# Optimization experiments

Hardware: AMD Instinct MI355X
Metric: run time of the kernel (lower is better)

Reference implementation:

```python
import jax, jax.numpy as jnp
import numpy as np

EPS = 1e-5

def _offset_conv(x, w, b):
    # 3x3 conv, padding=1, producing 2*K*K offset channels (standard DeformConv2D v1)
    out = jax.lax.conv_general_dilated(x, w, (1, 1), ((1, 1), (1, 1)),
                                       dimension_numbers=('NCHW', 'OIHW', 'NCHW'))
    return out + b[None, :, None, None]

def _bilinear_gather(x, py, px):
    # x: [B,C,H,W]; py,px: [B,K2,H,W] float sample coords -> [B,C,K2,H,W]
    B, C, H, W = x.shape
    py = jnp.clip(py, 0.0, H - 1.0)
    px = jnp.clip(px, 0.0, W - 1.0)
    y0 = jnp.floor(py)
    x0 = jnp.floor(px)
    wy = py - y0
    wx = px - x0
    y0i = y0.astype(jnp.int32)
    x0i = x0.astype(jnp.int32)
    y1i = jnp.minimum(y0i + 1, H - 1)
    x1i = jnp.minimum(x0i + 1, W - 1)
    xf = x.reshape(B, C, H * W)
    K2, Ho, Wo = py.shape[1], py.shape[2], py.shape[3]
    def gather(yy, xx):
        idx = (yy * W + xx).reshape(B, 1, -1)  # broadcast over C
        return jnp.take_along_axis(xf, idx, axis=2).reshape(B, C, K2, Ho, Wo)
    v00 = gather(y0i, x0i)
    v01 = gather(y0i, x1i)
    v10 = gather(y1i, x0i)
    v11 = gather(y1i, x1i)
    wy = wy[:, None]
    wx = wx[:, None]
    return (v00 * (1 - wy) * (1 - wx) + v01 * (1 - wy) * wx
            + v10 * wy * (1 - wx) + v11 * wy * wx)

def _deform_dw(x, w_off, b_off, w_dw, k):
    # depthwise deformable conv, kernel k, padding k//2 (same spatial size)
    B, C, H, W = x.shape
    K2 = k * k
    off = _offset_conv(x, w_off, b_off)      # [B, 2*K2, H, W]
    dy, dx = off[:, :K2], off[:, K2:]
    r = (k - 1) // 2
    pn = jnp.arange(-r, r + 1, dtype=x.dtype)
    pn_y = jnp.repeat(pn, k)[None, :, None, None]  # [1,K2,1,1]
    pn_x = jnp.tile(pn, k)[None, :, None, None]
    gy = jnp.arange(H, dtype=x.dtype)[None, None, :, None]
    gx = jnp.arange(W, dtype=x.dtype)[None, None, None, :]
    py = gy + pn_y + dy
    px = gx + pn_x + dx
    samp = _bilinear_gather(x, py, px)        # [B,C,K2,H,W]
    return jnp.einsum('bckhw,ck->bchw', samp, w_dw.reshape(C, K2))

def _bn_relu(x, g, b, m, v):
    inv = g / jnp.sqrt(v + EPS)
    return jax.nn.relu(x * inv[None, :, None, None] + (b - m * inv)[None, :, None, None])

def setup_inputs() -> dict:
    key = jax.random.key(0)
    B, C, H, W, O = 4, 96, 64, 64, 192
    ks = jax.random.split(key, 32)
    d = {'x': jax.random.normal(ks[0], (B, C, H, W), jnp.float32)}
    i = 1
    for k in (3, 5, 7):
        K2 = k * k
        d[f'w_off{k}'] = 0.01 * jax.random.normal(ks[i], (2 * K2, C, 3, 3), jnp.float32); i += 1
        d[f'b_off{k}'] = jnp.zeros((2 * K2,), jnp.float32)
        d[f'w_dw{k}'] = jax.random.normal(ks[i], (C, k, k), jnp.float32) / k; i += 1
        d[f'g{k}'] = jnp.ones((C,), jnp.float32)
        d[f'be{k}'] = jnp.zeros((C,), jnp.float32)
        d[f'm{k}'] = 0.1 * jax.random.normal(ks[i], (C,), jnp.float32); i += 1
        d[f'v{k}'] = jax.random.uniform(ks[i], (C,), jnp.float32, 0.5, 1.5); i += 1
    d['w_pw'] = jax.random.normal(ks[i], (O, 3 * C), jnp.float32) / np.sqrt(3 * C).astype(np.float32); i += 1
    d['gp'] = jnp.ones((O,), jnp.float32)
    d['bp'] = jnp.zeros((O,), jnp.float32)
    d['mp'] = 0.1 * jax.random.normal(ks[i], (O,), jnp.float32); i += 1
    d['vp'] = jax.random.uniform(ks[i], (O,), jnp.float32, 0.5, 1.5)
    return d

def reference(x, w_off3, b_off3, w_dw3, g3, be3, m3, v3,
              w_off5, b_off5, w_dw5, g5, be5, m5, v5,
              w_off7, b_off7, w_dw7, g7, be7, m7, v7,
              w_pw, gp, bp, mp, vp):
    x1 = _bn_relu(_deform_dw(x, w_off3, b_off3, w_dw3, 3), g3, be3, m3, v3)
    x2 = _bn_relu(_deform_dw(x, w_off5, b_off5, w_dw5, 5), g5, be5, m5, v5)
    x3 = _bn_relu(_deform_dw(x, w_off7, b_off7, w_dw7, 7), g7, be7, m7, v7)
    xc = jnp.concatenate([x1, x2, x3], axis=1)  # [B, 3C, H, W]
    out = jnp.einsum('bchw,oc->bohw', xc, w_pw)  # 1x1 conv
    return _bn_relu(out, gp, bp, mp, vp)
```

## Files before the change

### kernel.cpp

```cpp
#include <hip/hip_runtime.h>
#include <hip/hip_fp16.h>
#include <math.h>

typedef unsigned short u16;
typedef _Float16 f16x8 __attribute__((ext_vector_type(8)));
typedef float f32x4 __attribute__((ext_vector_type(4)));

#define HWp 4096
#define Cc 96
#define Bb 4
#define Oo 192
#define C3 288

#define OFF_WDWT  0
#define OFF_BCAT  14112
#define OFF_SBR   14304
#define OFF_HBR   14592
#define OFF_SPW   14880
#define OFF_HPW   15072
#define FP32_END  15264
#define BF_XTPAD  0
#define BF_WOF    1672704
#define BF_WPW    1838592

__device__ __forceinline__ u16 f2h(float f) { return __half_as_ushort(__float2half(f)); }
__device__ __forceinline__ float h2f(u16 u) { union { __half h; u16 u; } t; t.u = u; return __half2float(t.h); }
__device__ __forceinline__ unsigned h2u(__half2 h) { union { __half2 h; unsigned u; } t; t.h = h; return t.u; }
__device__ __forceinline__ __half2 u2h(unsigned u) { union { __half2 h; unsigned u; } t; t.u = u; return t.h; }

#define PREP_N (165888 + 55296 + 14112 + 192 + 288 + 288 + 192 + 192 + 24960)
#define PREP_BLK ((PREP_N + 255) / 256)

__global__ __launch_bounds__(256) void prep_kernel(
    const float* __restrict__ x,
    const float* __restrict__ w3, const float* __restrict__ b3, const float* __restrict__ dw3,
    const float* __restrict__ g3, const float* __restrict__ be3, const float* __restrict__ m3, const float* __restrict__ v3,
    const float* __restrict__ w5, const float* __restrict__ b5, const float* __restrict__ dw5,
    const float* __restrict__ g5, const float* __restrict__ be5, const float* __restrict__ m5, const float* __restrict__ v5,
    const float* __restrict__ w7, const float* __restrict__ b7, const float* __restrict__ dw7,
    const float* __restrict__ g7, const float* __restrict__ be7, const float* __restrict__ m7, const float* __restrict__ v7,
    const float* __restrict__ wpw,
    const float* __restrict__ gp, const float* __restrict__ bp, const float* __restrict__ mp, const float* __restrict__ vp,
    float* __restrict__ ws)
{
    __shared__ u16 sT[64 * 104];
    u16* bf = (u16*)(ws + FP32_END);
    const int tid = threadIdx.x;

    if (blockIdx.x < 256) {
        const int b = blockIdx.x >> 6, h = blockIdx.x & 63;
        const float* xb = x + (((size_t)b * Cc) << 12) + (h << 6);
#pragma unroll
        for (int it = 0; it < 24; ++it) {
            int j = tid + it * 256;
            int c = j >> 6, p = j & 63;
            sT[p * 104 + c] = f2h(xb[((size_t)c << 12) + p]);
        }
        __syncthreads();
        u16* dst = bf + BF_XTPAD + ((size_t)(b * 66 + h + 1) * 66 + 1) * 96;
#pragma unroll
        for (int it = 0; it < 6; ++it) {
            int j = tid + it * 256;
            int pos = j / 24, c4 = j % 24;
            const u16* s = &sT[pos * 104 + c4 * 4];
            *(uint2*)(dst + pos * 96 + c4 * 4) = make_uint2(
                (unsigned)s[0] | ((unsigned)s[1] << 16),
                (unsigned)s[2] | ((unsigned)s[3] << 16));
        }
        return;
    }

    int i = (blockIdx.x - 256) * 256 + tid;
    if (i < 165888) {
        int f = i / 13824, r = i % 13824;
        int s = r >> 9, l = r & 511;
        int lane = l >> 3, j = l & 7;
        int o = f * 16 + (lane & 15);
        int k = s * 32 + (lane >> 4) * 8 + j;
        int tap = k / 96, c = k % 96;
        float v = 0.f;
        if (o < 18)       v = w3[o * 864 + c * 9 + tap];
        else if (o < 68)  v = w5[(o - 18) * 864 + c * 9 + tap];
        else if (o < 166) v = w7[(o - 68) * 864 + c * 9 + tap];
        bf[BF_WOF + i] = f2h(v);
        return;
    }
    int j = i - 165888;
    if (j < 55296) {
        int f = j / 4608, r = j % 4608;
        int s = r >> 9, l = r & 511;
        int lane = l >> 3, jj = l & 7;
        int o = f * 16 + (lane & 15);
        int k = s * 32 + (lane >> 4) * 8 + jj;
        bf[BF_WPW + j] = f2h(wpw[o * C3 + k]);
        return;
    }
    j -= 55296;
    if (j < 14112) {
        int ksel = j / 4704, rem = j % 4704;
        int t = rem / 96, c = rem % 96;
        int K2 = (ksel == 0) ? 9 : (ksel == 1) ? 25 : 49;
        const float* dw = (ksel == 0) ? dw3 : (ksel == 1) ? dw5 : dw7;
        ws[OFF_WDWT + j] = (t < K2) ? dw[c * K2 + t] : 0.f;
        return;
    }
    j -= 14112;
    if (j < 192) {
        float v = 0.f;
        if (j < 18)       v = b3[j];
        else if (j < 68)  v = b5[j - 18];
        else if (j < 166) v = b7[j - 68];
        ws[OFF_BCAT + j] = v;
        return;
    }
    j -= 192;
    if (j < C3) {
        int ks = j / Cc, c = j % Cc;
        const float* g = (ks == 0) ? g3 : (ks == 1) ? g5 : g7;
        const float* v = (ks == 0) ? v3 : (ks == 1) ? v5 : v7;
        ws[OFF_SBR + j] = g[c] / sqrtf(v[c] + 1e-5f);
        return;
    }
    j -= C3;
    if (j < C3) {
        int ks = j / Cc, c = j % Cc;
        const float* g = (ks == 0) ? g3 : (ks == 1) ? g5 : g7;
        const float* v = (ks == 0) ? v3 : (ks == 1) ? v5 : v7;
        const float* be = (ks == 0) ? be3 : (ks == 1) ? be5 : be7;
        const float* m = (ks == 0) ? m3 : (ks == 1) ? m5 : m7;
        float inv = g[c] / sqrtf(v[c] + 1e-5f);
        ws[OFF_HBR + j] = be[c] - m[c] * inv;
        return;
    }
    j -= C3;
    if (j < Oo) { ws[OFF_SPW + j] = gp[j] / sqrtf(vp[j] + 1e-5f); return; }
    j -= Oo;
    if (j < Oo) {
        float inv = gp[j] / sqrtf(vp[j] + 1e-5f);
        ws[OFF_HPW + j] = bp[j] - mp[j] * inv;
        return;
    }
    j -= Oo;
    if (j < 24960) {
        int c4 = j % 24, rem = j / 24;
        int cell = rem % 260, bb = rem / 260;
        int row, col;
        if (cell < 66)       { row = 0;  col = cell; }
        else if (cell < 132) { row = 65; col = cell - 66; }
        else if (cell < 196) { row = cell - 132 + 1; col = 0; }
        else                 { row = cell - 196 + 1; col = 65; }
        u16* dst = bf + BF_XTPAD + ((size_t)(bb * 66 + row) * 66 + col) * 96 + c4 * 4;
        *(uint2*)dst = make_uint2(0u, 0u);
        return;
    }
}

#define GATHER_TAP(SEG, T, GT) do {                                          \
    const uint4 e = sWI[((GT) << 4) + q];                                    \
    const __half2 wAh = u2h(e.x), wBh = u2h(e.y);                            \
    const __half2 w00b = __low2half2(wAh), w01b = __high2half2(wAh);         \
    const __half2 w10b = __low2half2(wBh), w11b = __high2half2(wBh);         \
    const unsigned d01 = e.w & 0xffffu, d10 = e.w >> 16;                     \
    const uint4 u00 = *(const uint4*)(xcb + e.z);                            \
    const uint4 u01 = *(const uint4*)(xcb + e.z + d01);                      \
    const uint4 u10 = *(const uint4*)(xcb + e.z + d10);                      \
    const uint4 u11 = *(const uint4*)(xcb + e.z + d10 + d01);                \
    const float4 wda = *(const float4*)(wdT##SEG + (T) * 96);                \
    const float4 wdb = *(const float4*)(wdT##SEG + (T) * 96 + 4);            \
    const unsigned a00[4] = {u00.x, u00.y, u00.z, u00.w};                    \
    const unsigned a01[4] = {u01.x, u01.y, u01.z, u01.w};                    \
    const unsigned a10[4] = {u10.x, u10.y, u10.z, u10.w};                    \
    const unsigned a11[4] = {u11.x, u11.y, u11.z, u11.w};                    \
    const float wd[8] = {wda.x, wda.y, wda.z, wda.w, wdb.x, wdb.y, wdb.z, wdb.w}; \
    _Pragma("unroll")                                                        \
    for (int d = 0; d < 4; ++d) {                                            \
        __half2 v = __hmul2(w00b, u2h(a00[d]));                              \
        v = __hfma2(w01b, u2h(a01[d]), v);                                   \
        v = __hfma2(w10b, u2h(a10[d]), v);                                   \
        v = __hfma2(w11b, u2h(a11[d]), v);                                   \
        acc##SEG[2 * d]     = fmaf(wd[2 * d],     __low2float(v),  acc##SEG[2 * d]);     \
        acc##SEG[2 * d + 1] = fmaf(wd[2 * d + 1], __high2float(v), acc##SEG[2 * d + 1]); \
    }                                                                        \
} while (0)

#define SEG_EPI(SEG) do {                                                    \
    const int cb = (SEG) * Cc + c;                                           \
    const float4 sa = *(const float4*)(ws + OFF_SBR + cb);                   \
    const float4 sb = *(const float4*)(ws + OFF_SBR + cb + 4);               \
    const float4 ha = *(const float4*)(ws + OFF_HBR + cb);                   \
    const float4 hb = *(const float4*)(ws + OFF_HBR + cb + 4);               \
    const float ss[8] = {sa.x, sa.y, sa.z, sa.w, sb.x, sb.y, sb.z, sb.w};    \
    const float hh8[8] = {ha.x, ha.y, ha.z, ha.w, hb.x, hb.y, hb.z, hb.w};   \
    unsigned rr[4];                                                          \
    _Pragma("unroll")                                                        \
    for (int d = 0; d < 4; ++d) {                                            \
        float lo = fmaxf(fmaf(acc##SEG[2 * d],     ss[2 * d],     hh8[2 * d]),     0.f); \
        float hi = fmaxf(fmaf(acc##SEG[2 * d + 1], ss[2 * d + 1], hh8[2 * d + 1]), 0.f); \
        rr[d] = h2u(__floats2half2_rn(lo, hi));                              \
    }                                                                        \
    *(uint4*)(ytile + q * 296 + cb) = make_uint4(rr[0], rr[1], rr[2], rr[3]); \
} while (0)

__global__ __launch_bounds__(256, 4) void mega_kernel(
    const float* __restrict__ ws, float* __restrict__ out)
{
    __shared__ uint4 regA[1328];
    __shared__ u16  regB[4736];
    u16* sX = (u16*)regA;
    uint4* sWI = regA;
    u16* soff = regB;
    u16* ytile = regB;

    const u16* bf = (const u16*)(ws + FP32_END);
    const u16* xp = bf + BF_XTPAD;
    const int tid = threadIdx.x;
    const int lane = tid & 63, wid = tid >> 6;
    const int lane15 = lane & 15, quad = lane >> 4;

    const int bx = blockIdx.x;
    const int xcd = bx & 7;
    const int b = xcd >> 1;
    const int tile = ((bx >> 3) << 1) + (xcd & 1);
    const int p0 = tile * 16;
    const int h = p0 >> 6;
    const int w0 = p0 & 63;

    {
        const u16* src = xp + ((size_t)(b * 66 + h) * 66 + w0) * 96;
        for (int j = tid; j < 1296; j += 256) {
            int r = j / 432;
            int rem = j % 432;
            int col = rem / 24, c4 = rem % 24;
            uint2 v = *(const uint2*)(src + ((size_t)(r * 66 + col)) * 96 + c4 * 4);
            *(uint2*)(&sX[(r * 18 + col) * 104 + c4 * 4]) = v;
        }
    }
    __syncthreads();

    {
        const u16* wof = bf + BF_WOF;
        f32x4 acc[3];
#pragma unroll
        for (int ff = 0; ff < 3; ++ff) acc[ff] = (f32x4){0.f, 0.f, 0.f, 0.f};
#pragma unroll
        for (int tap = 0; tap < 9; ++tap) {
            const int ky2 = tap / 3, kx2 = tap % 3;
            const u16* brow = &sX[(ky2 * 18 + kx2 + lane15) * 104 + quad * 8];
#pragma unroll
            for (int cc = 0; cc < 3; ++cc) {
                f16x8 bb = *(const f16x8*)(brow + cc * 32);
                const int s = tap * 3 + cc;
#pragma unroll
                for (int ff = 0; ff < 3; ++ff) {
                    const int f = wid * 3 + ff;
                    f16x8 a = *(const f16x8*)(wof + ((size_t)(f * 27 + s) * 64 + lane) * 8);
                    acc[ff] = __builtin_amdgcn_mfma_f32_16x16x32_f16(a, bb, acc[ff], 0, 0, 0);
                }
            }
        }
        const float* bcat = ws + OFF_BCAT;
#pragma unroll
        for (int ff = 0; ff < 3; ++ff) {
#pragma unroll
            for (int r = 0; r < 4; ++r) {
                int co = (wid * 3 + ff) * 16 + quad * 4 + r;
                soff[co * 16 + lane15] = f2h(acc[ff][r] + bcat[co]);
            }
        }
    }
    __syncthreads();

    for (int i = tid; i < 1328; i += 256) {
        int gt = i >> 4, q = i & 15;
        int K, K2, R, tb, t;
        if (gt < 9)       { K = 3; K2 = 9;  R = 1; tb = 0;  t = gt; }
        else if (gt < 34) { K = 5; K2 = 25; R = 2; tb = 18; t = gt - 9; }
        else              { K = 7; K2 = 49; R = 3; tb = 68; t = gt - 34; }
        int ky = t / K - R, kx = t % K - R;
        float dy = h2f(soff[(tb + t) * 16 + q]);
        float dx = h2f(soff[(tb + K2 + t) * 16 + q]);
        float py = fminf(fmaxf((float)(h + ky) + dy, 0.f), 63.f);
        float px = fminf(fmaxf((float)(w0 + q + kx) + dx, 0.f), 63.f);
        float fy = floorf(py), fx = floorf(px);
        int y0 = (int)fy, x0 = (int)fx;
        float wy = py - fy, wx = px - fx;
        int y1 = min(y0 + 1, 63), x1 = min(x0 + 1, 63);
        float w11 = wy * wx;
        float w10 = wy - w11;
        float w01 = wx - w11;
        float w00 = 1.f - wy - wx + w11;
        unsigned wA = h2u(__floats2half2_rn(w00, w01));
        unsigned wB = h2u(__floats2half2_rn(w10, w11));
        unsigned o00 = (unsigned)((y0 + 1) * 66 + (x0 + 1)) * 192u;
        unsigned d01 = (unsigned)(x1 - x0) * 192u;
        unsigned d10 = (unsigned)(y1 - y0) * 12672u;
        sWI[i] = make_uint4(wA, wB, o00, d01 | (d10 << 16));
    }
    __syncthreads();

    if (tid < 192) {
        const int c8 = tid % 12;
        const int q  = tid / 12;
        const int c = c8 * 8;
        const u16* xh = xp + (size_t)b * 66 * 66 * 96;
        const char* xcb = (const char*)xh + c * 2;
        const float* wdT0 = ws + OFF_WDWT + 0 * 4704 + c;
        const float* wdT1 = ws + OFF_WDWT + 1 * 4704 + c;
        const float* wdT2 = ws + OFF_WDWT + 2 * 4704 + c;

        float acc0[8], acc1[8], acc2[8];
#pragma unroll
        for (int k = 0; k < 8; ++k) { acc0[k] = 0.f; acc1[k] = 0.f; acc2[k] = 0.f; }

#pragma unroll
        for (int ky = -3; ky <= 3; ++ky) {
            if (ky >= -1 && ky <= 1) {
#pragma unroll
                for (int kx = -1; kx <= 1; ++kx) {
                    const int t = (ky + 1) * 3 + (kx + 1);
                    GATHER_TAP(0, t, t);
                }
            }
            if (ky >= -2 && ky <= 2) {
#pragma unroll
                for (int kx = -2; kx <= 2; ++kx) {
                    const int t = (ky + 2) * 5 + (kx + 2);
                    GATHER_TAP(1, t, 9 + t);
                }
            }
#pragma unroll
            for (int kx = -3; kx <= 3; ++kx) {
                const int t = (ky + 3) * 7 + (kx + 3);
                GATHER_TAP(2, t, 34 + t);
            }
        }

        SEG_EPI(0);
        SEG_EPI(1);
        SEG_EPI(2);
    }
    __syncthreads();

    {
        const u16* wpw = bf + BF_WPW;
        f32x4 acc[3];
#pragma unroll
        for (int ff = 0; ff < 3; ++ff) acc[ff] = (f32x4){0.f, 0.f, 0.f, 0.f};
        const u16* brow = &ytile[lane15 * 296 + quad * 8];
#pragma unroll
        for (int s = 0; s < 9; ++s) {
            f16x8 bb = *(const f16x8*)(brow + s * 32);
#pragma unroll
            for (int ff = 0; ff < 3; ++ff) {
                const int f = wid * 3 + ff;
                f16x8 a = *(const f16x8*)(wpw + ((size_t)(f * 9 + s) * 64 + lane) * 8);
                acc[ff] = __builtin_amdgcn_mfma_f32_16x16x32_f16(a, bb, acc[ff], 0, 0, 0);
            }
        }
        const float* spw = ws + OFF_SPW;
        const float* hpw = ws + OFF_HPW;
        const int p = p0 + lane15;
#pragma unroll
        for (int ff = 0; ff < 3; ++ff) {
#pragma unroll
            for (int r = 0; r < 4; ++r) {
                int o = (wid * 3 + ff) * 16 + quad * 4 + r;
                out[(((size_t)(b * Oo + o)) << 12) + p] =
                    fmaxf(fmaf(acc[ff][r], spw[o], hpw[o]), 0.f);
            }
        }
    }
}

extern "C" void kernel_launch(void* const* d_in, const int* in_sizes, int n_in,
                              void* d_out, int out_size, void* d_ws, size_t ws_size,
                              hipStream_t stream)
{
    const float* x     = (const float*)d_in[0];
    const float* w3    = (const float*)d_in[1];
    const float* b3    = (const float*)d_in[2];
    const float* dw3   = (const float*)d_in[3];
    const float* g3    = (const float*)d_in[4];
    const float* be3   = (const float*)d_in[5];
    const float* m3    = (const float*)d_in[6];
    const float* v3    = (const float*)d_in[7];
    const float* w5    = (const float*)d_in[8];
    const float* b5    = (const float*)d_in[9];
    const float* dw5   = (const float*)d_in[10];
    const float* g5    = (const float*)d_in[11];
    const float* be5   = (const float*)d_in[12];
    const float* m5    = (const float*)d_in[13];
    const float* v5    = (const float*)d_in[14];
    const float* w7    = (const float*)d_in[15];
    const float* b7    = (const float*)d_in[16];
    const float* dw7   = (const float*)d_in[17];
    const float* g7    = (const float*)d_in[18];
    const float* be7   = (const float*)d_in[19];
    const float* m7    = (const float*)d_in[20];
    const float* v7    = (const float*)d_in[21];
    const float* wpw   = (const float*)d_in[22];
    const float* gp    = (const float*)d_in[23];
    const float* bp    = (const float*)d_in[24];
    const float* mp    = (const float*)d_in[25];
    const float* vp    = (const float*)d_in[26];

    float* ws = (float*)d_ws;
    float* out = (float*)d_out;

    {
        prep_kernel<<<256 + PREP_BLK, 256, 0, stream>>>(
            x,
            w3, b3, dw3, g3, be3, m3, v3,
            w5, b5, dw5, g5, be5, m5, v5,
            w7, b7, dw7, g7, be7, m7, v7,
            wpw, gp, bp, mp, vp, ws);
    }
    {
        mega_kernel<<<1024, 256, 0, stream>>>(ws, out);
    }
}
```

Before: 177.3 us.

## Pad channels to 128 and software-pipeline deformable gather across all threads

Pads the channel stride of the transposed input and depthwise weights from 96 to 128 so that all 256 threads, as 16 channel groups by 16 pixels, take part in the bilinear gather instead of only 192. Per-kernel-size segments now run sequentially with one accumulator set, and the next tap's four gathered values are prefetched before the current tap's FMA. The aim is better load-latency hiding and lower register pressure. The cost is about a third more padded memory traffic, and a quarter of the threads do wasted work on zero padding channels.

```diff
diff --git a/kernel.cpp b/kernel.cpp
--- a/kernel.cpp
+++ b/kernel.cpp
@@ -13,22 +13,22 @@
 #define C3 288
 
 #define OFF_WDWT  0
-#define OFF_BCAT  14112
-#define OFF_SBR   14304
-#define OFF_HBR   14592
-#define OFF_SPW   14880
-#define OFF_HPW   15072
-#define FP32_END  15264
+#define OFF_BCAT  18816
+#define OFF_SBR   19008
+#define OFF_HBR   19296
+#define OFF_SPW   19584
+#define OFF_HPW   19776
+#define FP32_END  19968
 #define BF_XTPAD  0
-#define BF_WOF    1672704
-#define BF_WPW    1838592
+#define BF_WOF    2230272
+#define BF_WPW    2396160
 
 __device__ __forceinline__ u16 f2h(float f) { return __half_as_ushort(__float2half(f)); }
 __device__ __forceinline__ float h2f(u16 u) { union { __half h; u16 u; } t; t.u = u; return __half2float(t.h); }
 __device__ __forceinline__ unsigned h2u(__half2 h) { union { __half2 h; unsigned u; } t; t.h = h; return t.u; }
 __device__ __forceinline__ __half2 u2h(unsigned u) { union { __half2 h; unsigned u; } t; t.u = u; return t.h; }
 
-#define PREP_N (165888 + 55296 + 14112 + 192 + 288 + 288 + 192 + 192 + 24960)
+#define PREP_N (165888 + 55296 + 18816 + 192 + 288 + 288 + 192 + 192 + 33280)
 #define PREP_BLK ((PREP_N + 255) / 256)
 
 __global__ __launch_bounds__(256) void prep_kernel(
@@ -57,15 +57,21 @@
             sT[p * 104 + c] = f2h(xb[((size_t)c << 12) + p]);
         }
         __syncthreads();
-        u16* dst = bf + BF_XTPAD + ((size_t)(b * 66 + h + 1) * 66 + 1) * 96;
+        u16* dst = bf + BF_XTPAD + ((size_t)(b * 66 + h + 1) * 66 + 1) * 128;
 #pragma unroll
         for (int it = 0; it < 6; ++it) {
             int j = tid + it * 256;
             int pos = j / 24, c4 = j % 24;
             const u16* s = &sT[pos * 104 + c4 * 4];
-            *(uint2*)(dst + pos * 96 + c4 * 4) = make_uint2(
+            *(uint2*)(dst + pos * 128 + c4 * 4) = make_uint2(
                 (unsigned)s[0] | ((unsigned)s[1] << 16),
                 (unsigned)s[2] | ((unsigned)s[3] << 16));
+        }
+#pragma unroll
+        for (int it = 0; it < 2; ++it) {
+            int j = tid + it * 256;
+            int pos = j >> 3, g = j & 7;
+            *(uint2*)(dst + pos * 128 + 96 + g * 4) = make_uint2(0u, 0u);
         }
         return;
     }
@@ -96,15 +102,15 @@
         return;
     }
     j -= 55296;
-    if (j < 14112) {
-        int ksel = j / 4704, rem = j % 4704;
-        int t = rem / 96, c = rem % 96;
+    if (j < 18816) {
+        int ksel = j / 6272, rem = j % 6272;
+        int t = rem / 128, c = rem % 128;
         int K2 = (ksel == 0) ? 9 : (ksel == 1) ? 25 : 49;
         const float* dw = (ksel == 0) ? dw3 : (ksel == 1) ? dw5 : dw7;
-        ws[OFF_WDWT + j] = (t < K2) ? dw[c * K2 + t] : 0.f;
-        return;
-    }
-    j -= 14112;
+        ws[OFF_WDWT + j] = (t < K2 && c < 96) ? dw[c * K2 + t] : 0.f;
+        return;
+    }
+    j -= 18816;
     if (j < 192) {
         float v = 0.f;
         if (j < 18)       v = b3[j];
@@ -141,64 +147,81 @@
         return;
     }
     j -= Oo;
-    if (j < 24960) {
-        int c4 = j % 24, rem = j / 24;
+    if (j < 33280) {
+        int c4 = j % 32, rem = j / 32;
         int cell = rem % 260, bb = rem / 260;
         int row, col;
         if (cell < 66)       { row = 0;  col = cell; }
         else if (cell < 132) { row = 65; col = cell - 66; }
         else if (cell < 196) { row = cell - 132 + 1; col = 0; }
         else                 { row = cell - 196 + 1; col = 65; }
-        u16* dst = bf + BF_XTPAD + ((size_t)(bb * 66 + row) * 66 + col) * 96 + c4 * 4;
+        u16* dst = bf + BF_XTPAD + ((size_t)(bb * 66 + row) * 66 + col) * 128 + c4 * 4;
         *(uint2*)dst = make_uint2(0u, 0u);
         return;
     }
 }
 
-#define GATHER_TAP(SEG, T, GT) do {                                          \
-    const uint4 e = sWI[((GT) << 4) + q];                                    \
-    const __half2 wAh = u2h(e.x), wBh = u2h(e.y);                            \
+#define TAP_FMA(E, U00, U01, U10, U11, WD, ACC) do {                         \
+    const __half2 wAh = u2h((E).x), wBh = u2h((E).y);                        \
     const __half2 w00b = __low2half2(wAh), w01b = __high2half2(wAh);         \
     const __half2 w10b = __low2half2(wBh), w11b = __high2half2(wBh);         \
-    const unsigned d01 = e.w & 0xffffu, d10 = e.w >> 16;                     \
-    const uint4 u00 = *(const uint4*)(xcb + e.z);                            \
-    const uint4 u01 = *(const uint4*)(xcb + e.z + d01);                      \
-    const uint4 u10 = *(const uint4*)(xcb + e.z + d10);                      \
-    const uint4 u11 = *(const uint4*)(xcb + e.z + d10 + d01);                \
-    const float4 wda = *(const float4*)(wdT##SEG + (T) * 96);                \
-    const float4 wdb = *(const float4*)(wdT##SEG + (T) * 96 + 4);            \
-    const unsigned a00[4] = {u00.x, u00.y, u00.z, u00.w};                    \
-    const unsigned a01[4] = {u01.x, u01.y, u01.z, u01.w};                    \
-    const unsigned a10[4] = {u10.x, u10.y, u10.z, u10.w};                    \
-    const unsigned a11[4] = {u11.x, u11.y, u11.z, u11.w};                    \
-    const float wd[8] = {wda.x, wda.y, wda.z, wda.w, wdb.x, wdb.y, wdb.z, wdb.w}; \
+    const unsigned a00[4] = {(U00).x, (U00).y, (U00).z, (U00).w};            \
+    const unsigned a01[4] = {(U01).x, (U01).y, (U01).z, (U01).w};            \
+    const unsigned a10[4] = {(U10).x, (U10).y, (U10).z, (U10).w};            \
+    const unsigned a11[4] = {(U11).x, (U11).y, (U11).z, (U11).w};            \
     _Pragma("unroll")                                                        \
     for (int d = 0; d < 4; ++d) {                                            \
         __half2 v = __hmul2(w00b, u2h(a00[d]));                              \
         v = __hfma2(w01b, u2h(a01[d]), v);                                   \
         v = __hfma2(w10b, u2h(a10[d]), v);                                   \
         v = __hfma2(w11b, u2h(a11[d]), v);                                   \
-        acc##SEG[2 * d]     = fmaf(wd[2 * d],     __low2float(v),  acc##SEG[2 * d]);     \
-        acc##SEG[2 * d + 1] = fmaf(wd[2 * d + 1], __high2float(v), acc##SEG[2 * d + 1]); \
+        (ACC)[2 * d]     = fmaf((WD)[2 * d],     __low2float(v),  (ACC)[2 * d]);     \
+        (ACC)[2 * d + 1] = fmaf((WD)[2 * d + 1], __high2float(v), (ACC)[2 * d + 1]); \
     }                                                                        \
 } while (0)
 
-#define SEG_EPI(SEG) do {                                                    \
-    const int cb = (SEG) * Cc + c;                                           \
-    const float4 sa = *(const float4*)(ws + OFF_SBR + cb);                   \
-    const float4 sb = *(const float4*)(ws + OFF_SBR + cb + 4);               \
-    const float4 ha = *(const float4*)(ws + OFF_HBR + cb);                   \
-    const float4 hb = *(const float4*)(ws + OFF_HBR + cb + 4);               \
-    const float ss[8] = {sa.x, sa.y, sa.z, sa.w, sb.x, sb.y, sb.z, sb.w};    \
-    const float hh8[8] = {ha.x, ha.y, ha.z, ha.w, hb.x, hb.y, hb.z, hb.w};   \
-    unsigned rr[4];                                                          \
+#define SEG_LOOP(SEG, K2v, GB) do {                                          \
+    const float* wdT = ws + OFF_WDWT + (SEG) * 6272 + c;                     \
+    float acc[8];                                                            \
+    _Pragma("unroll") for (int k = 0; k < 8; ++k) acc[k] = 0.f;              \
+    uint4 e = sWI[((GB) << 4) + q];                                          \
+    uint4 u00 = *(const uint4*)(xcb + e.z);                                  \
+    uint4 u01 = *(const uint4*)(xcb + e.z + (e.w & 0xffffu));                \
+    uint4 u10 = *(const uint4*)(xcb + e.z + (e.w >> 16));                    \
+    uint4 u11 = *(const uint4*)(xcb + e.z + (e.w >> 16) + (e.w & 0xffffu));  \
     _Pragma("unroll")                                                        \
-    for (int d = 0; d < 4; ++d) {                                            \
-        float lo = fmaxf(fmaf(acc##SEG[2 * d],     ss[2 * d],     hh8[2 * d]),     0.f); \
-        float hi = fmaxf(fmaf(acc##SEG[2 * d + 1], ss[2 * d + 1], hh8[2 * d + 1]), 0.f); \
-        rr[d] = h2u(__floats2half2_rn(lo, hi));                              \
+    for (int t = 0; t < (K2v); ++t) {                                        \
+        uint4 e2, v00, v01, v10, v11;                                        \
+        if (t + 1 < (K2v)) {                                                 \
+            e2 = sWI[(((GB) + t + 1) << 4) + q];                             \
+            v00 = *(const uint4*)(xcb + e2.z);                               \
+            v01 = *(const uint4*)(xcb + e2.z + (e2.w & 0xffffu));            \
+            v10 = *(const uint4*)(xcb + e2.z + (e2.w >> 16));                \
+            v11 = *(const uint4*)(xcb + e2.z + (e2.w >> 16) + (e2.w & 0xffffu)); \
+        }                                                                    \
+        const float4 wda = *(const float4*)(wdT + t * 128);                  \
+        const float4 wdb = *(const float4*)(wdT + t * 128 + 4);              \
+        const float wd[8] = {wda.x, wda.y, wda.z, wda.w, wdb.x, wdb.y, wdb.z, wdb.w}; \
+        TAP_FMA(e, u00, u01, u10, u11, wd, acc);                             \
+        e = e2; u00 = v00; u01 = v01; u10 = v10; u11 = v11;                  \
     }                                                                        \
-    *(uint4*)(ytile + q * 296 + cb) = make_uint4(rr[0], rr[1], rr[2], rr[3]); \
+    if (cg < 12) {                                                           \
+        const int cb = (SEG) * Cc + c;                                       \
+        const float4 sa = *(const float4*)(ws + OFF_SBR + cb);               \
+        const float4 sb = *(const float4*)(ws + OFF_SBR + cb + 4);           \
+        const float4 ha = *(const float4*)(ws + OFF_HBR + cb);               \
+        const float4 hb = *(const float4*)(ws + OFF_HBR + cb + 4);           \
+        const float ss[8] = {sa.x, sa.y, sa.z, sa.w, sb.x, sb.y, sb.z, sb.w};\
+        const float hh8[8] = {ha.x, ha.y, ha.z, ha.w, hb.x, hb.y, hb.z, hb.w};\
+        unsigned rr[4];                                                      \
+        _Pragma("unroll")                                                    \
+        for (int d = 0; d < 4; ++d) {                                        \
+            float lo = fmaxf(fmaf(acc[2 * d],     ss[2 * d],     hh8[2 * d]),     0.f); \
+            float hi = fmaxf(fmaf(acc[2 * d + 1], ss[2 * d + 1], hh8[2 * d + 1]), 0.f); \
+            rr[d] = h2u(__floats2half2_rn(lo, hi));                          \
+        }                                                                    \
+        *(uint4*)(ytile + q * 296 + cb) = make_uint4(rr[0], rr[1], rr[2], rr[3]); \
+    }                                                                        \
 } while (0)
 
 __global__ __launch_bounds__(256, 4) void mega_kernel(
@@ -226,12 +249,12 @@
     const int w0 = p0 & 63;
 
     {
-        const u16* src = xp + ((size_t)(b * 66 + h) * 66 + w0) * 96;
+        const u16* src = xp + ((size_t)(b * 66 + h) * 66 + w0) * 128;
         for (int j = tid; j < 1296; j += 256) {
             int r = j / 432;
             int rem = j % 432;
             int col = rem / 24, c4 = rem % 24;
-            uint2 v = *(const uint2*)(src + ((size_t)(r * 66 + col)) * 96 + c4 * 4);
+            uint2 v = *(const uint2*)(src + ((size_t)(r * 66 + col)) * 128 + c4 * 4);
             *(uint2*)(&sX[(r * 18 + col) * 104 + c4 * 4]) = v;
         }
     }
@@ -291,53 +314,23 @@
         float w00 = 1.f - wy - wx + w11;
         unsigned wA = h2u(__floats2half2_rn(w00, w01));
         unsigned wB = h2u(__floats2half2_rn(w10, w11));
-        unsigned o00 = (unsigned)((y0 + 1) * 66 + (x0 + 1)) * 192u;
-        unsigned d01 = (unsigned)(x1 - x0) * 192u;
-        unsigned d10 = (unsigned)(y1 - y0) * 12672u;
+        unsigned o00 = (unsigned)((y0 + 1) * 66 + (x0 + 1)) * 256u;
+        unsigned d01 = (unsigned)(x1 - x0) * 256u;
+        unsigned d10 = (unsigned)(y1 - y0) * 16896u;
         sWI[i] = make_uint4(wA, wB, o00, d01 | (d10 << 16));
     }
     __syncthreads();
 
-    if (tid < 192) {
-        const int c8 = tid % 12;
-        const int q  = tid / 12;
-        const int c = c8 * 8;
-        const u16* xh = xp + (size_t)b * 66 * 66 * 96;
+    {
+        const int cg = tid & 15;
+        const int q  = tid >> 4;
+        const int c  = cg * 8;
+        const u16* xh = xp + (size_t)b * 66 * 66 * 128;
         const char* xcb = (const char*)xh + c * 2;
-        const float* wdT0 = ws + OFF_WDWT + 0 * 4704 + c;
-        const float* wdT1 = ws + OFF_WDWT + 1 * 4704 + c;
-        const float* wdT2 = ws + OFF_WDWT + 2 * 4704 + c;
-
-        float acc0[8], acc1[8], acc2[8];
-#pragma unroll
-        for (int k = 0; k < 8; ++k) { acc0[k] = 0.f; acc1[k] = 0.f; acc2[k] = 0.f; }
-
-#pragma unroll
-        for (int ky = -3; ky <= 3; ++ky) {
-            if (ky >= -1 && ky <= 1) {
-#pragma unroll
-                for (int kx = -1; kx <= 1; ++kx) {
-                    const int t = (ky + 1) * 3 + (kx + 1);
-                    GATHER_TAP(0, t, t);
-                }
-            }
-            if (ky >= -2 && ky <= 2) {
-#pragma unroll
-                for (int kx = -2; kx <= 2; ++kx) {
-                    const int t = (ky + 2) * 5 + (kx + 2);
-                    GATHER_TAP(1, t, 9 + t);
-                }
-            }
-#pragma unroll
-            for (int kx = -3; kx <= 3; ++kx) {
-                const int t = (ky + 3) * 7 + (kx + 3);
-                GATHER_TAP(2, t, 34 + t);
-            }
-        }
-
-        SEG_EPI(0);
-        SEG_EPI(1);
-        SEG_EPI(2);
+
+        SEG_LOOP(0, 9, 0);
+        SEG_LOOP(1, 25, 9);
+        SEG_LOOP(2, 49, 34);
     }
     __syncthreads();
 
```

Result: slower. 505.8 us (+185.3%).
